# Performance work log

Measured on AMD Instinct MI355X. Metric: run time of the kernel, lower is better.

## Reference

```python
import jax, jax.numpy as jnp
import numpy as np

D = 512      # feature_dim
DK = 64      # key_feature_dim
LQ = 2048
LK = 2048
B = 16
EPS = 1e-9


def _l2norm(x, axis=-1, eps=1e-12):
    # matches torch F.normalize(p=2): x / max(||x||, eps)
    n = jnp.sqrt(jnp.sum(x * x, axis=axis, keepdims=True))
    return x / jnp.maximum(n, eps)


def setup_inputs() -> dict:
    key = jax.random.key(0)
    ks = jax.random.split(key, 7)
    std = np.sqrt(2.0 / DK)
    stdv = np.sqrt(2.0 / D)
    return {
        "query": jax.random.normal(ks[0], (LQ, B, D), jnp.float32),
        "key": jax.random.normal(ks[1], (LK, B, D), jnp.float32),
        "value": jax.random.normal(ks[2], (LK, B, D), jnp.float32),
        "WK": jax.random.normal(ks[3], (DK, D), jnp.float32) * std,
        "WQ": jax.random.normal(ks[4], (DK, D), jnp.float32) * std,
        "WV": jax.random.normal(ks[5], (D, D), jnp.float32) * stdv,
        "Wt": jax.random.normal(ks[6], (D, D), jnp.float32) * (1.0 / np.sqrt(D)),  # trans_conv weight
    }


def reference(query, key, value, WK, WQ, WV, Wt):
    # q/k projections + cosine normalization; tensors are [L, B, *]
    w_k = _l2norm(key @ WK.T)      # [LK, B, DK]
    w_q = _l2norm(query @ WQ.T)    # [LQ, B, DK]
    # dot_prod: [B, LQ, LK]
    dot = jnp.einsum('qbd,kbd->bqk', w_q, w_k)
    affinity = jax.nn.softmax(dot, axis=-1)  # temp = 1
    # second renorm over the query axis (dim=1)
    affinity = affinity / (EPS + jnp.sum(affinity, axis=1, keepdims=True))
    w_v = value @ WV.T                        # [LK, B, D]
    out = jnp.einsum('bqk,kbd->qbd', affinity, w_v)  # [LQ, B, D]
    out = (query - out) @ Wt.T
    return jax.nn.relu(out)
```

## Files before the change

### kernel.cpp

```cpp
#include <hip/hip_runtime.h>

#define LQ 2048
#define LK 2048
#define BB 16
#define DD 512
#define DKK 64
#define EPSF 1e-9f

typedef unsigned short u16;
typedef unsigned char u8;
typedef long i64;
typedef __attribute__((ext_vector_type(8))) short bf16x8;
typedef __attribute__((ext_vector_type(4))) float f32x4;
#define MFMA16(a, b, c) __builtin_amdgcn_mfma_f32_16x16x32_bf16(a, b, c, 0, 0, 0)
#define MFMAF8(a, b, c) __builtin_amdgcn_mfma_f32_16x16x32_fp8_fp8(a, b, c, 0, 0, 0)

__device__ inline u16 f2bf(float f) {
    unsigned int u = __float_as_uint(f);
    u += 0x7fffu + ((u >> 16) & 1u);
    return (u16)(u >> 16);
}
__device__ inline bf16x8 cvt8(float4 a, float4 b) {
    bf16x8 r;
    r[0] = (short)f2bf(a.x); r[1] = (short)f2bf(a.y); r[2] = (short)f2bf(a.z); r[3] = (short)f2bf(a.w);
    r[4] = (short)f2bf(b.x); r[5] = (short)f2bf(b.y); r[6] = (short)f2bf(b.z); r[7] = (short)f2bf(b.w);
    return r;
}
__device__ inline int pk_fp8x4(float a, float b, float c, float d) {
    int r = __builtin_amdgcn_cvt_pk_fp8_f32(a, b, 0, false);
    r = __builtin_amdgcn_cvt_pk_fp8_f32(c, d, r, true);
    return r;
}
__device__ inline void gload16(const void* g, void* l) {
    __builtin_amdgcn_global_load_lds((const __attribute__((address_space(1))) unsigned int*)g,
                                     (__attribute__((address_space(3))) unsigned int*)l, 16, 0, 0);
}

__global__ __launch_bounds__(256) void k_cvt(const float* __restrict__ src, u16* __restrict__ dst, int n) {
    int i = (blockIdx.x * 256 + threadIdx.x) * 4;
    if (i < n) {
        float4 v = *reinterpret_cast<const float4*>(src + i);
        *reinterpret_cast<ushort4*>(dst + i) = make_ushort4(f2bf(v.x), f2bf(v.y), f2bf(v.z), f2bf(v.w));
    }
}

__global__ __launch_bounds__(256) void k_cvtv(const float* __restrict__ value, u16* __restrict__ vb) {
    size_t i = ((size_t)blockIdx.x * 256 + threadIdx.x) * 8;
    int k = (int)(i >> 13);
    int r = (int)(i & 8191);
    int b = r >> 9, d = r & 511;
    float4 a = *reinterpret_cast<const float4*>(value + i);
    float4 c = *reinterpret_cast<const float4*>(value + i + 4);
    *reinterpret_cast<bf16x8*>(vb + ((size_t)b * LK + k) * DD + d) = cvt8(a, c);
}

__global__ __launch_bounds__(256) void k_projqk(const float* __restrict__ xq, const float* __restrict__ xk,
                                                const u16* __restrict__ Wq, const u16* __restrict__ Wk,
                                                u16* __restrict__ yq, u16* __restrict__ yk)
{
    const float* x = blockIdx.z ? xk : xq;
    const u16* Wb = blockIdx.z ? Wk : Wq;
    u16* y = blockIdx.z ? yk : yq;
    const int b = blockIdx.y, r0 = blockIdx.x * 64;
    const int tid = threadIdx.x, wave = tid >> 6, lane = tid & 63, l15 = lane & 15, g = lane >> 4;
    const int rw = r0 + wave * 16;
    f32x4 z = {0.f, 0.f, 0.f, 0.f};
    f32x4 acc[4];
#pragma unroll
    for (int nf = 0; nf < 4; nf++) acc[nf] = z;

    for (int kt = 0; kt < DD; kt += 32) {
        const float* p = x + ((size_t)(rw + l15) * BB + b) * DD + kt + g * 8;
        bf16x8 af = cvt8(*reinterpret_cast<const float4*>(p), *reinterpret_cast<const float4*>(p + 4));
#pragma unroll
        for (int nf = 0; nf < 4; nf++) {
            bf16x8 bf_ = *reinterpret_cast<const bf16x8*>(Wb + (size_t)(nf * 16 + l15) * DD + kt + g * 8);
            acc[nf] = MFMA16(af, bf_, acc[nf]);
        }
    }
    float rn[4];
#pragma unroll
    for (int j = 0; j < 4; j++) {
        float t2 = acc[0][j] * acc[0][j] + acc[1][j] * acc[1][j]
                 + acc[2][j] * acc[2][j] + acc[3][j] * acc[3][j];
        t2 += __shfl_xor(t2, 1, 64);
        t2 += __shfl_xor(t2, 2, 64);
        t2 += __shfl_xor(t2, 4, 64);
        t2 += __shfl_xor(t2, 8, 64);
        rn[j] = 1.f / fmaxf(sqrtf(t2), 1e-12f);
    }
#pragma unroll
    for (int nf = 0; nf < 4; nf++)
#pragma unroll
        for (int j = 0; j < 4; j++) {
            int q = rw + g * 4 + j;
            y[((size_t)b * LQ + q) * DKK + nf * 16 + l15] = f2bf(acc[nf][j] * rn[j]);
        }
}

__global__ __launch_bounds__(256) void k_score(const u16* __restrict__ wqb, const u16* __restrict__ wkb,
                                               u8* __restrict__ E0, float* __restrict__ Rpart, int b0)
{
    const int kb = blockIdx.x, c = blockIdx.y, bl = blockIdx.z, b = b0 + bl;
    const int tid = threadIdx.x, wave = tid >> 6, lane = tid & 63, l15 = lane & 15, g = lane >> 4;
    const int k0 = kb * 64;
    f32x4 z = {0.f, 0.f, 0.f, 0.f};

    const u16* ar = wkb + ((size_t)b * LK + k0 + wave * 16 + l15) * DKK;
    bf16x8 af0 = *reinterpret_cast<const bf16x8*>(ar + g * 8);
    bf16x8 af1 = *reinterpret_cast<const bf16x8*>(ar + 32 + g * 8);
    u8* Eb = E0 + (size_t)bl * LQ * LK;
    float* Rp = Rpart + ((size_t)bl * 128 + kb * 4 + wave) * LQ;

    for (int ct = 0; ct < 512; ct += 64) {
#pragma unroll
        for (int n = 0; n < 4; n++) {
            int q = c * 512 + ct + n * 16 + l15;
            const u16* br = wqb + ((size_t)b * LQ + q) * DKK;
            bf16x8 b0v = *reinterpret_cast<const bf16x8*>(br + g * 8);
            bf16x8 b1v = *reinterpret_cast<const bf16x8*>(br + 32 + g * 8);
            f32x4 s = z;
            s = MFMA16(af0, b0v, s);
            s = MFMA16(af1, b1v, s);
            float pe[4];
#pragma unroll
            for (int j = 0; j < 4; j++) pe[j] = __expf(s[j]);
            *reinterpret_cast<int*>(Eb + (size_t)q * LK + k0 + wave * 16 + g * 4) =
                pk_fp8x4(pe[0], pe[1], pe[2], pe[3]);
            float v = pe[0] + pe[1] + pe[2] + pe[3];
            v += __shfl_xor(v, 16, 64);
            v += __shfl_xor(v, 32, 64);
            if (g == 0) Rp[q] = v;
        }
    }
}

__global__ __launch_bounds__(256) void k_rsum(const float* __restrict__ Rpart, float* __restrict__ Rq, int b0) {
    int idx = blockIdx.x * 256 + threadIdx.x;
    int bl = idx >> 11, q = idx & 2047;
    const float* rp = Rpart + (size_t)bl * 128 * LQ + q;
    float s = 0.f;
    for (int p = 0; p < 128; p++) s += rp[(size_t)p * LQ];
    Rq[(size_t)(b0 + bl) * LQ + q] = 1.f / s;
}

__global__ __launch_bounds__(256) void k_colsum(const u8* __restrict__ E0, const float* __restrict__ Rq,
                                                float* __restrict__ Cpart, int b0)
{
    const int kc = blockIdx.x, qc = blockIdx.y, bl = blockIdx.z;
    const int tid = threadIdx.x, sub = tid >> 6, lane = tid & 63;
    const u8* Eb = E0 + (size_t)bl * LQ * LK + (size_t)kc * 1024 + lane * 16;
    const float* rq = Rq + (size_t)(b0 + bl) * LQ + qc * 128;
    float acc[16];
#pragma unroll
    for (int i = 0; i < 16; i++) acc[i] = 0.f;
    for (int qi = 0; qi < 32; qi++) {
        int q = qi * 4 + sub;
        uint4 raw = *reinterpret_cast<const uint4*>(Eb + (size_t)(qc * 128 + q) * LK);
        float w = rq[q];
        const unsigned int* rw = (const unsigned int*)&raw;
#pragma unroll
        for (int dw = 0; dw < 4; dw++) {
            unsigned int u = rw[dw];
#pragma unroll
            for (int by = 0; by < 4; by++) {
                unsigned int f = 0x3C000000u + (((u >> (8 * by)) & 0x7Fu) << 20);
                acc[dw * 4 + by] += __uint_as_float(f) * w;
            }
        }
    }
    __shared__ float red[4][64][16];
#pragma unroll
    for (int i = 0; i < 16; i++) red[sub][lane][i] = acc[i];
    __syncthreads();
    if (sub == 0) {
#pragma unroll
        for (int i = 0; i < 16; i++) {
            float v = red[0][lane][i] + red[1][lane][i] + red[2][lane][i] + red[3][lane][i];
            Cpart[((size_t)bl * 16 + qc) * LK + kc * 1024 + lane * 16 + i] = v;
        }
    }
}

__global__ __launch_bounds__(256) void k_csum(const float* __restrict__ Cpart, float* __restrict__ ci, int b0) {
    int idx = blockIdx.x * 256 + threadIdx.x;
    int bl = idx >> 11, k = idx & 2047;
    const float* cp = Cpart + (size_t)bl * 16 * LK + k;
    float s = 0.f;
#pragma unroll
    for (int p = 0; p < 16; p++) s += cp[(size_t)p * LK];
    ci[(size_t)(b0 + bl) * LK + k] = 1.f / (EPSF + s);
}

__global__ __launch_bounds__(256, 3) void k_projv(const u16* __restrict__ vb, const u16* __restrict__ WVb,
                                                  const float* __restrict__ ci, u8* __restrict__ wvS, int b0)
{
    const int b = b0 + blockIdx.z, k0 = blockIdx.x * 128, n0 = blockIdx.y * 128;
    const int tid = threadIdx.x, wv = tid >> 6, lane = tid & 63, l15 = lane & 15, g = lane >> 4;
    const int qg = wv >> 1, dg = wv & 1;

    __shared__ __align__(16) u16 As[128 * 64], Bs[128 * 64];

    const int srow = wv * 8 + (lane >> 3);
    const int scb = ((lane & 7) * 16) ^ ((srow & 7) << 4);
    const char* gA = (const char*)(vb + ((size_t)b * LK + k0 + srow) * DD) + scb;
    const char* gB = (const char*)(WVb + (size_t)(n0 + srow) * DD) + scb;
    const size_t rstep = (size_t)32 * DD * 2;

    f32x4 z = {0.f, 0.f, 0.f, 0.f};
    f32x4 acc[4][4];
#pragma unroll
    for (int m = 0; m < 4; m++)
#pragma unroll
        for (int nf = 0; nf < 4; nf++) acc[m][nf] = z;

#pragma unroll
    for (int p = 0; p < 4; ++p) {
        gload16(gA + p * rstep, (char*)As + p * 4096 + wv * 1024);
        gload16(gB + p * rstep, (char*)Bs + p * 4096 + wv * 1024);
    }

    for (int tt = 0; tt < DD / 64; ++tt) {
        __syncthreads();
        bf16x8 af[4][2], bv[4][2];
#pragma unroll
        for (int m = 0; m < 4; m++) {
            int row = qg * 64 + m * 16 + l15;
            const char* rp = (const char*)As + row * 128;
            int x = (row & 7) << 4;
#pragma unroll
            for (int kk = 0; kk < 2; kk++)
                af[m][kk] = *reinterpret_cast<const bf16x8*>(rp + ((kk * 64 + g * 16) ^ x));
        }
#pragma unroll
        for (int nf = 0; nf < 4; nf++) {
            int row = dg * 64 + nf * 16 + l15;
            const char* rp = (const char*)Bs + row * 128;
            int x = (row & 7) << 4;
#pragma unroll
            for (int kk = 0; kk < 2; kk++)
                bv[nf][kk] = *reinterpret_cast<const bf16x8*>(rp + ((kk * 64 + g * 16) ^ x));
        }
        __syncthreads();
        if (tt + 1 < DD / 64) {
            int ktb = (tt + 1) * 128;
#pragma unroll
            for (int p = 0; p < 4; ++p) {
                gload16(gA + p * rstep + ktb, (char*)As + p * 4096 + wv * 1024);
                gload16(gB + p * rstep + ktb, (char*)Bs + p * 4096 + wv * 1024);
            }
        }
#pragma unroll
        for (int nf = 0; nf < 4; nf++)
#pragma unroll
            for (int m = 0; m < 4; m++) {
                acc[m][nf] = MFMA16(af[m][0], bv[nf][0], acc[m][nf]);
                acc[m][nf] = MFMA16(af[m][1], bv[nf][1], acc[m][nf]);
            }
    }
#pragma unroll
    for (int m = 0; m < 4; m++) {
        float cv[4];
        int kb = k0 + qg * 64 + m * 16 + g * 4;
#pragma unroll
        for (int j = 0; j < 4; j++) cv[j] = ci[(size_t)b * LK + kb + j];
#pragma unroll
        for (int nf = 0; nf < 4; nf++) {
            int d = n0 + dg * 64 + nf * 16 + l15;
            *reinterpret_cast<int*>(wvS + ((size_t)b * DD + d) * LK + kb) =
                pk_fp8x4(acc[m][nf][0] * cv[0], acc[m][nf][1] * cv[1],
                         acc[m][nf][2] * cv[2], acc[m][nf][3] * cv[3]);
        }
    }
}

__global__ __launch_bounds__(256, 3) void k_pvgemm(const float* __restrict__ query,
                                                   const u8* __restrict__ E0,
                                                   const u8* __restrict__ wvS,
                                                   const float* __restrict__ Rq,
                                                   u16* __restrict__ tout, int b0, int G)
{
    const int i = blockIdx.x;
    int bl, tile;
    if (G == 16) { bl = (i & 7) + 8 * (i >> 9); tile = (i >> 3) & 63; }
    else         { bl = i % G; tile = i / G; }
    const int b = b0 + bl;
    const int q0 = (tile >> 2) * 128, n0 = (tile & 3) * 128;
    const int tid = threadIdx.x, wv = tid >> 6, lane = tid & 63, l15 = lane & 15, g = lane >> 4;
    const int qg = wv >> 1, dg = wv & 1;

    __shared__ __align__(16) char As[16384], Bs[16384];

    const u8* Eb = E0 + (size_t)bl * LQ * LK;
    const u8* Vb = wvS + (size_t)b * DD * LK;

    const int srow = wv * 8 + (lane >> 3);
    const int scb = ((lane & 7) * 16) ^ ((srow & 7) << 4);
    const char* gA = (const char*)Eb + (size_t)(q0 + srow) * LK + scb;
    const char* gB = (const char*)Vb + (size_t)(n0 + srow) * LK + scb;
    const size_t rstep = (size_t)32 * LK;

    f32x4 z = {0.f, 0.f, 0.f, 0.f};
    f32x4 acc[4][4];
#pragma unroll
    for (int m = 0; m < 4; m++)
#pragma unroll
        for (int nf = 0; nf < 4; nf++) acc[m][nf] = z;

    auto stage = [&](int t) {
#pragma unroll
        for (int p = 0; p < 4; ++p) {
            gload16(gA + p * rstep + t * 128, (char*)As + p * 4096 + wv * 1024);
            gload16(gB + p * rstep + t * 128, (char*)Bs + p * 4096 + wv * 1024);
        }
    };
    stage(0);

    for (int t = 0; t < LK / 128; ++t) {
        __syncthreads();
        i64 af[4][4], bv[4][4];
#pragma unroll
        for (int m = 0; m < 4; m++) {
            int row = qg * 64 + m * 16 + l15;
            const char* rp = (const char*)As + row * 128;
            int x = (row & 7) << 4;
#pragma unroll
            for (int kk = 0; kk < 4; kk++)
                af[m][kk] = *reinterpret_cast<const i64*>(rp + ((kk * 32 + g * 8) ^ x));
        }
#pragma unroll
        for (int nf = 0; nf < 4; nf++) {
            int row = dg * 64 + nf * 16 + l15;
            const char* rp = (const char*)Bs + row * 128;
            int x = (row & 7) << 4;
#pragma unroll
            for (int kk = 0; kk < 4; kk++)
                bv[nf][kk] = *reinterpret_cast<const i64*>(rp + ((kk * 32 + g * 8) ^ x));
        }
        __syncthreads();
        if (t + 1 < LK / 128) stage(t + 1);
#pragma unroll
        for (int kk = 0; kk < 4; kk++)
#pragma unroll
            for (int nf = 0; nf < 4; nf++)
#pragma unroll
                for (int m = 0; m < 4; m++)
                    acc[m][nf] = MFMAF8(af[m][kk], bv[nf][kk], acc[m][nf]);
    }
#pragma unroll
    for (int m = 0; m < 4; m++) {
        float rqv[4];
#pragma unroll
        for (int j = 0; j < 4; j++)
            rqv[j] = Rq[(size_t)b * LQ + q0 + qg * 64 + m * 16 + g * 4 + j];
#pragma unroll
        for (int nf = 0; nf < 4; nf++)
#pragma unroll
            for (int j = 0; j < 4; j++) {
                int q = q0 + qg * 64 + m * 16 + g * 4 + j;
                int d = n0 + dg * 64 + nf * 16 + l15;
                size_t idx = ((size_t)q * BB + b) * DD + d;
                tout[idx] = f2bf(query[idx] - acc[m][nf][j] * rqv[j]);
            }
    }
}

__global__ __launch_bounds__(256, 3) void k_final(const u16* __restrict__ t, const u16* __restrict__ Wtb,
                                                  float* __restrict__ out)
{
    const int r0 = blockIdx.x * 128, n0 = blockIdx.y * 128;
    const int tid = threadIdx.x, wv = tid >> 6, lane = tid & 63, l15 = lane & 15, g = lane >> 4;
    const int qg = wv >> 1, dg = wv & 1;

    __shared__ __align__(16) u16 As[128 * 64], Bs[128 * 64];

    const int srow = wv * 8 + (lane >> 3);
    const int scb = ((lane & 7) * 16) ^ ((srow & 7) << 4);
    const char* gA = (const char*)(t + (size_t)(r0 + srow) * DD) + scb;
    const char* gB = (const char*)(Wtb + (size_t)(n0 + srow) * DD) + scb;
    const size_t rstep = (size_t)32 * DD * 2;

    f32x4 z = {0.f, 0.f, 0.f, 0.f};
    f32x4 acc[4][4];
#pragma unroll
    for (int m = 0; m < 4; m++)
#pragma unroll
        for (int nf = 0; nf < 4; nf++) acc[m][nf] = z;

#pragma unroll
    for (int p = 0; p < 4; ++p) {
        gload16(gA + p * rstep, (char*)As + p * 4096 + wv * 1024);
        gload16(gB + p * rstep, (char*)Bs + p * 4096 + wv * 1024);
    }

    for (int tt = 0; tt < DD / 64; ++tt) {
        __syncthreads();
        bf16x8 af[4][2], bv[4][2];
#pragma unroll
        for (int m = 0; m < 4; m++) {
            int row = qg * 64 + m * 16 + l15;
            const char* rp = (const char*)As + row * 128;
            int x = (row & 7) << 4;
#pragma unroll
            for (int kk = 0; kk < 2; kk++)
                af[m][kk] = *reinterpret_cast<const bf16x8*>(rp + ((kk * 64 + g * 16) ^ x));
        }
#pragma unroll
        for (int nf = 0; nf < 4; nf++) {
            int row = dg * 64 + nf * 16 + l15;
            const char* rp = (const char*)Bs + row * 128;
            int x = (row & 7) << 4;
#pragma unroll
            for (int kk = 0; kk < 2; kk++)
                bv[nf][kk] = *reinterpret_cast<const bf16x8*>(rp + ((kk * 64 + g * 16) ^ x));
        }
        __syncthreads();
        if (tt + 1 < DD / 64) {
            int ktb = (tt + 1) * 128;
#pragma unroll
            for (int p = 0; p < 4; ++p) {
                gload16(gA + p * rstep + ktb, (char*)As + p * 4096 + wv * 1024);
                gload16(gB + p * rstep + ktb, (char*)Bs + p * 4096 + wv * 1024);
            }
        }
#pragma unroll
        for (int nf = 0; nf < 4; nf++)
#pragma unroll
            for (int m = 0; m < 4; m++) {
                acc[m][nf] = MFMA16(af[m][0], bv[nf][0], acc[m][nf]);
                acc[m][nf] = MFMA16(af[m][1], bv[nf][1], acc[m][nf]);
            }
    }
#pragma unroll
    for (int m = 0; m < 4; m++)
#pragma unroll
        for (int nf = 0; nf < 4; nf++)
#pragma unroll
            for (int j = 0; j < 4; j++)
                out[(size_t)(r0 + qg * 64 + m * 16 + g * 4 + j) * DD + n0 + dg * 64 + nf * 16 + l15] =
                    fmaxf(acc[m][nf][j], 0.f);
}

extern "C" void kernel_launch(void* const* d_in, const int* in_sizes, int n_in,
                              void* d_out, int out_size, void* d_ws, size_t ws_size,
                              hipStream_t stream)
{
    const float* query = (const float*)d_in[0];
    const float* key   = (const float*)d_in[1];
    const float* value = (const float*)d_in[2];
    const float* WK    = (const float*)d_in[3];
    const float* WQ    = (const float*)d_in[4];
    const float* WV    = (const float*)d_in[5];
    const float* Wt    = (const float*)d_in[6];
    float* out = (float*)d_out;

    char* ws = (char*)d_ws;
    u16*   wqb = (u16*)(ws);
    u16*   wkb = (u16*)(ws + (4u << 20));
    u8*    wvS = (u8*)(ws + (8u << 20));
    u16*   t   = (u16*)(ws + (24u << 20));
    u16*   vb  = (u16*)(ws + (56u << 20));
    float* Rq  = (float*)(ws + (88u << 20));
    float* ci  = (float*)(ws + (88u << 20) + (128u << 10));
    u16*   WQb = (u16*)(ws + (88u << 20) + (256u << 10));
    u16*   WKb = (u16*)(ws + (88u << 20) + (320u << 10));
    u16*   WVb = (u16*)(ws + (88u << 20) + (384u << 10));
    u16*   Wtb = (u16*)(ws + (88u << 20) + (896u << 10));

    const size_t fixed = 90ull << 20;
    const size_t perG = (4ull << 20) + (1ull << 20) + (128ull << 10);
    int G = 0;
    for (int g = 16; g >= 1; g >>= 1)
        if (fixed + (size_t)g * perG <= ws_size) { G = g; break; }
    if (G == 0) G = 1;
    u8*    E0    = (u8*)(ws + fixed);
    float* Rpart = (float*)(ws + fixed + ((size_t)G << 22));
    float* Cpart = (float*)(ws + fixed + ((size_t)G << 22) + ((size_t)G << 20));

    k_cvt<<<32, 256, 0, stream>>>(WQ, WQb, DKK * DD);
    k_cvt<<<32, 256, 0, stream>>>(WK, WKb, DKK * DD);
    k_cvt<<<256, 256, 0, stream>>>(WV, WVb, DD * DD);
    k_cvt<<<256, 256, 0, stream>>>(Wt, Wtb, DD * DD);
    k_cvtv<<<8192, 256, 0, stream>>>(value, vb);

    k_projqk<<<dim3(LQ / 64, BB, 2), 256, 0, stream>>>(query, key, WQb, WKb, wqb, wkb);

    for (int b0 = 0; b0 < BB; b0 += G) {
        k_score<<<dim3(LK / 64, LQ / 512, G), 256, 0, stream>>>(wqb, wkb, E0, Rpart, b0);
        k_rsum<<<G * 8, 256, 0, stream>>>(Rpart, Rq, b0);
        k_colsum<<<dim3(2, 16, G), 256, 0, stream>>>(E0, Rq, Cpart, b0);
        k_csum<<<G * 8, 256, 0, stream>>>(Cpart, ci, b0);
        k_projv<<<dim3(LK / 128, DD / 128, G), 256, 0, stream>>>(vb, WVb, ci, wvS, b0);
        k_pvgemm<<<64 * G, 256, 0, stream>>>(query, E0, wvS, Rq, t, b0, G);
    }

    k_final<<<dim3(LQ * BB / 128, DD / 128), 256, 0, stream>>>(t, Wtb, out);
}
```

Before: 303.6 us.

## Store exp-score matrix in MFMA-fragment tiled layout for score, colsum and PV

```diff
diff --git a/kernel.cpp b/kernel.cpp
--- a/kernel.cpp
+++ b/kernel.cpp
@@ -99,39 +99,38 @@
 }
 
 __global__ __launch_bounds__(256) void k_score(const u16* __restrict__ wqb, const u16* __restrict__ wkb,
-                                               u8* __restrict__ E0, float* __restrict__ Rpart, int b0)
-{
-    const int kb = blockIdx.x, c = blockIdx.y, bl = blockIdx.z, b = b0 + bl;
-    const int tid = threadIdx.x, wave = tid >> 6, lane = tid & 63, l15 = lane & 15, g = lane >> 4;
-    const int k0 = kb * 64;
+                                               u8* __restrict__ E0t, float* __restrict__ Rpart, int b0)
+{
+    const int kb = blockIdx.x, qc = blockIdx.y, bl = blockIdx.z, b = b0 + bl;
+    const int tid = threadIdx.x, w = tid >> 6, lane = tid & 63, l15 = lane & 15, g = lane >> 4;
+    const int k0 = kb * 64, kt = kb * 4 + w;
     f32x4 z = {0.f, 0.f, 0.f, 0.f};
 
-    const u16* ar = wkb + ((size_t)b * LK + k0 + wave * 16 + l15) * DKK;
+    const u16* ar = wkb + ((size_t)b * LK + k0 + w * 16 + l15) * DKK;
     bf16x8 af0 = *reinterpret_cast<const bf16x8*>(ar + g * 8);
     bf16x8 af1 = *reinterpret_cast<const bf16x8*>(ar + 32 + g * 8);
-    u8* Eb = E0 + (size_t)bl * LQ * LK;
-    float* Rp = Rpart + ((size_t)bl * 128 + kb * 4 + wave) * LQ;
-
-    for (int ct = 0; ct < 512; ct += 64) {
-#pragma unroll
-        for (int n = 0; n < 4; n++) {
-            int q = c * 512 + ct + n * 16 + l15;
-            const u16* br = wqb + ((size_t)b * LQ + q) * DKK;
-            bf16x8 b0v = *reinterpret_cast<const bf16x8*>(br + g * 8);
-            bf16x8 b1v = *reinterpret_cast<const bf16x8*>(br + 32 + g * 8);
-            f32x4 s = z;
-            s = MFMA16(af0, b0v, s);
-            s = MFMA16(af1, b1v, s);
-            float pe[4];
-#pragma unroll
-            for (int j = 0; j < 4; j++) pe[j] = __expf(s[j]);
-            *reinterpret_cast<int*>(Eb + (size_t)q * LK + k0 + wave * 16 + g * 4) =
-                pk_fp8x4(pe[0], pe[1], pe[2], pe[3]);
-            float v = pe[0] + pe[1] + pe[2] + pe[3];
-            v += __shfl_xor(v, 16, 64);
-            v += __shfl_xor(v, 32, 64);
-            if (g == 0) Rp[q] = v;
-        }
+    u8* Eb = E0t + (size_t)bl * LQ * LK;
+    float* Rp = Rpart + ((size_t)bl * 128 + kt) * LQ;
+
+#pragma unroll 4
+    for (int qf = 0; qf < 32; qf++) {
+        int qt = qc * 32 + qf;
+        int q = qt * 16 + l15;
+        const u16* br = wqb + ((size_t)b * LQ + q) * DKK;
+        bf16x8 b0v = *reinterpret_cast<const bf16x8*>(br + g * 8);
+        bf16x8 b1v = *reinterpret_cast<const bf16x8*>(br + 32 + g * 8);
+        f32x4 s = z;
+        s = MFMA16(af0, b0v, s);
+        s = MFMA16(af1, b1v, s);
+        float pe[4];
+#pragma unroll
+        for (int j = 0; j < 4; j++) pe[j] = __expf(s[j]);
+        *reinterpret_cast<int*>(Eb + ((size_t)qt * 128 + kt) * 256 + l15 * 16 + g * 4) =
+            pk_fp8x4(pe[0], pe[1], pe[2], pe[3]);
+        float v = pe[0] + pe[1] + pe[2] + pe[3];
+        v += __shfl_xor(v, 16, 64);
+        v += __shfl_xor(v, 32, 64);
+        if (g == 0) Rp[q] = v;
     }
 }
 
@@ -144,51 +143,46 @@
     Rq[(size_t)(b0 + bl) * LQ + q] = 1.f / s;
 }
 
-__global__ __launch_bounds__(256) void k_colsum(const u8* __restrict__ E0, const float* __restrict__ Rq,
+__global__ __launch_bounds__(256) void k_colsum(const u8* __restrict__ E0t, const float* __restrict__ Rq,
                                                 float* __restrict__ Cpart, int b0)
 {
-    const int kc = blockIdx.x, qc = blockIdx.y, bl = blockIdx.z;
-    const int tid = threadIdx.x, sub = tid >> 6, lane = tid & 63;
-    const u8* Eb = E0 + (size_t)bl * LQ * LK + (size_t)kc * 1024 + lane * 16;
-    const float* rq = Rq + (size_t)(b0 + bl) * LQ + qc * 128;
-    float acc[16];
-#pragma unroll
-    for (int i = 0; i < 16; i++) acc[i] = 0.f;
-    for (int qi = 0; qi < 32; qi++) {
-        int q = qi * 4 + sub;
-        uint4 raw = *reinterpret_cast<const uint4*>(Eb + (size_t)(qc * 128 + q) * LK);
-        float w = rq[q];
-        const unsigned int* rw = (const unsigned int*)&raw;
-#pragma unroll
-        for (int dw = 0; dw < 4; dw++) {
-            unsigned int u = rw[dw];
-#pragma unroll
-            for (int by = 0; by < 4; by++) {
-                unsigned int f = 0x3C000000u + (((u >> (8 * by)) & 0x7Fu) << 20);
-                acc[dw * 4 + by] += __uint_as_float(f) * w;
-            }
-        }
-    }
-    __shared__ float red[4][64][16];
-#pragma unroll
-    for (int i = 0; i < 16; i++) red[sub][lane][i] = acc[i];
-    __syncthreads();
-    if (sub == 0) {
-#pragma unroll
-        for (int i = 0; i < 16; i++) {
-            float v = red[0][lane][i] + red[1][lane][i] + red[2][lane][i] + red[3][lane][i];
-            Cpart[((size_t)bl * 16 + qc) * LK + kc * 1024 + lane * 16 + i] = v;
-        }
+    const int qc = blockIdx.y, bl = blockIdx.z;
+    const int tid = threadIdx.x, w = tid >> 6, lane = tid & 63, l15 = lane & 15, g = lane >> 4;
+    const int kt = blockIdx.x * 4 + w;
+    const u8* base = E0t + (size_t)bl * LQ * LK + (size_t)kt * 256 + l15 * 16 + g * 4;
+    const float* rq = Rq + (size_t)(b0 + bl) * LQ;
+    float acc[4] = {0.f, 0.f, 0.f, 0.f};
+#pragma unroll 4
+    for (int i = 0; i < 32; i++) {
+        int qt = qc * 32 + i;
+        unsigned int u = *reinterpret_cast<const unsigned int*>(base + (size_t)qt * 32768);
+        float wgt = rq[qt * 16 + l15];
+#pragma unroll
+        for (int by = 0; by < 4; by++) {
+            unsigned int f = 0x3C000000u + (((u >> (8 * by)) & 0x7Fu) << 20);
+            acc[by] += __uint_as_float(f) * wgt;
+        }
+    }
+#pragma unroll
+    for (int by = 0; by < 4; by++) {
+        acc[by] += __shfl_xor(acc[by], 1, 64);
+        acc[by] += __shfl_xor(acc[by], 2, 64);
+        acc[by] += __shfl_xor(acc[by], 4, 64);
+        acc[by] += __shfl_xor(acc[by], 8, 64);
+    }
+    if (l15 == 0) {
+        float4 v4 = make_float4(acc[0], acc[1], acc[2], acc[3]);
+        *reinterpret_cast<float4*>(Cpart + ((size_t)bl * 4 + qc) * LK + kt * 16 + g * 4) = v4;
     }
 }
 
 __global__ __launch_bounds__(256) void k_csum(const float* __restrict__ Cpart, float* __restrict__ ci, int b0) {
     int idx = blockIdx.x * 256 + threadIdx.x;
     int bl = idx >> 11, k = idx & 2047;
-    const float* cp = Cpart + (size_t)bl * 16 * LK + k;
+    const float* cp = Cpart + (size_t)bl * 4 * LK + k;
     float s = 0.f;
 #pragma unroll
-    for (int p = 0; p < 16; p++) s += cp[(size_t)p * LK];
+    for (int p = 0; p < 4; p++) s += cp[(size_t)p * LK];
     ci[(size_t)(b0 + bl) * LK + k] = 1.f / (EPSF + s);
 }
 
@@ -275,7 +269,7 @@
 }
 
 __global__ __launch_bounds__(256, 3) void k_pvgemm(const float* __restrict__ query,
-                                                   const u8* __restrict__ E0,
+                                                   const u8* __restrict__ E0t,
                                                    const u8* __restrict__ wvS,
                                                    const float* __restrict__ Rq,
                                                    u16* __restrict__ tout, int b0, int G)
@@ -291,14 +285,14 @@
 
     __shared__ __align__(16) char As[16384], Bs[16384];
 
-    const u8* Eb = E0 + (size_t)bl * LQ * LK;
+    const u8* Eb = E0t + (size_t)bl * LQ * LK;
     const u8* Vb = wvS + (size_t)b * DD * LK;
 
+    const char* gAt = (const char*)Eb + (size_t)(q0 >> 4) * 128 * 256;
     const int srow = wv * 8 + (lane >> 3);
     const int scb = ((lane & 7) * 16) ^ ((srow & 7) << 4);
-    const char* gA = (const char*)Eb + (size_t)(q0 + srow) * LK + scb;
     const char* gB = (const char*)Vb + (size_t)(n0 + srow) * LK + scb;
-    const size_t rstep = (size_t)32 * LK;
+    const size_t rstepB = (size_t)32 * LK;
 
     f32x4 z = {0.f, 0.f, 0.f, 0.f};
     f32x4 acc[4][4];
@@ -310,8 +304,10 @@
     auto stage = [&](int t) {
 #pragma unroll
         for (int p = 0; p < 4; ++p) {
-            gload16(gA + p * rstep + t * 128, (char*)As + p * 4096 + wv * 1024);
-            gload16(gB + p * rstep + t * 128, (char*)Bs + p * 4096 + wv * 1024);
+            int c = wv * 4 + p;
+            gload16(gAt + ((size_t)(c >> 1) * 128 + t * 8) * 256 + (c & 1) * 1024 + lane * 16,
+                    (char*)As + c * 1024);
+            gload16(gB + p * rstepB + t * 128, (char*)Bs + p * 4096 + wv * 1024);
         }
     };
     stage(0);
@@ -321,12 +317,10 @@
         i64 af[4][4], bv[4][4];
 #pragma unroll
         for (int m = 0; m < 4; m++) {
-            int row = qg * 64 + m * 16 + l15;
-            const char* rp = (const char*)As + row * 128;
-            int x = (row & 7) << 4;
+            const char* rp = (const char*)As + (qg * 4 + m) * 2048 + l15 * 16 + (g & 1) * 8;
 #pragma unroll
             for (int kk = 0; kk < 4; kk++)
-                af[m][kk] = *reinterpret_cast<const i64*>(rp + ((kk * 32 + g * 8) ^ x));
+                af[m][kk] = *reinterpret_cast<const i64*>(rp + (kk * 2 + (g >> 1)) * 256);
         }
 #pragma unroll
         for (int nf = 0; nf < 4; nf++) {
@@ -468,7 +462,7 @@
     u16*   Wtb = (u16*)(ws + (88u << 20) + (896u << 10));
 
     const size_t fixed = 90ull << 20;
-    const size_t perG = (4ull << 20) + (1ull << 20) + (128ull << 10);
+    const size_t perG = (4ull << 20) + (1ull << 20) + (32ull << 10);
     int G = 0;
     for (int g = 16; g >= 1; g >>= 1)
         if (fixed + (size_t)g * perG <= ws_size) { G = g; break; }
@@ -488,7 +482,7 @@
     for (int b0 = 0; b0 < BB; b0 += G) {
         k_score<<<dim3(LK / 64, LQ / 512, G), 256, 0, stream>>>(wqb, wkb, E0, Rpart, b0);
         k_rsum<<<G * 8, 256, 0, stream>>>(Rpart, Rq, b0);
-        k_colsum<<<dim3(2, 16, G), 256, 0, stream>>>(E0, Rq, Cpart, b0);
+        k_colsum<<<dim3(32, 4, G), 256, 0, stream>>>(E0, Rq, Cpart, b0);
         k_csum<<<G * 8, 256, 0, stream>>>(Cpart, ci, b0);
         k_projv<<<dim3(LK / 128, DD / 128, G), 256, 0, stream>>>(vb, WVb, ci, wvS, b0);
         k_pvgemm<<<64 * G, 256, 0, stream>>>(query, E0, wvS, Rq, t, b0, G);
```

Measured after the change: 302.8 us. No clear change (-0.3%).
